# Optimization experiments

Hardware: AMD Instinct MI355X
Metric: run time of the kernel (lower is better)

## Reference

```python
import jax, jax.numpy as jnp
import numpy as np

N_NODES = 50000
D_IN = 128
D_OUT = 128
N_EDGES = 800000


def setup_inputs() -> dict:
    key = jax.random.key(0)
    ks = jax.random.split(key, 6)
    x = jax.random.normal(ks[0], (N_NODES, D_IN), dtype=jnp.float32)
    # xavier-uniform-ish init for the per-support weights
    limit = float(np.sqrt(6.0 / (D_IN + D_OUT)))
    weights = jax.random.uniform(ks[1], (2, D_IN, D_OUT), dtype=jnp.float32,
                                 minval=-limit, maxval=limit)
    edge_idx0 = jax.random.randint(ks[2], (2, N_EDGES), 0, N_NODES, dtype=jnp.int64 if jax.config.jax_enable_x64 else jnp.int32)
    vals0 = jax.random.uniform(ks[3], (N_EDGES,), dtype=jnp.float32)
    edge_idx1 = jax.random.randint(ks[4], (2, N_EDGES), 0, N_NODES, dtype=jnp.int64 if jax.config.jax_enable_x64 else jnp.int32)
    vals1 = jax.random.uniform(ks[5], (N_EDGES,), dtype=jnp.float32)
    return {"x": x, "weights": weights, "edge_idx0": edge_idx0, "vals0": vals0,
            "edge_idx1": edge_idx1, "vals1": vals1}


def _spmm(edge_idx, vals, dense, n_rows):
    # (sparse COO A) @ dense : out[row] += vals * dense[col]
    rows, cols = edge_idx[0], edge_idx[1]
    gathered = dense[cols] * vals[:, None]  # [E, D_OUT]
    return jax.ops.segment_sum(gathered, rows, num_segments=n_rows)


def reference(x, weights, edge_idx0, vals0, edge_idx1, vals1):
    n = x.shape[0]
    out = jnp.zeros((n, D_OUT), dtype=x.dtype)
    for w, ei, v in ((weights[0], edge_idx0, vals0), (weights[1], edge_idx1, vals1)):
        pre_sup = x @ w                       # [N, D_OUT] dense GEMM
        out = out + _spmm(ei, v, pre_sup, n)  # SpMM accumulate
    return jax.nn.relu(out)
```

## Files before the change

kernel.cpp:

```cpp
#include <hip/hip_runtime.h>

#define N_NODES 50000
#define D 128
#define N_EDGES 800000
#define SCAN_BLOCKS ((N_NODES + 255) / 256)
#define GEMM_BLOCKS ((N_NODES + 63) / 64)
#define BINS 196
#define NB1 256
#define CH1 3125
#define NKEY 2048

typedef __attribute__((ext_vector_type(8))) short short8;
typedef __attribute__((ext_vector_type(4))) float f32x4;

__device__ __forceinline__ unsigned short f2bf(float f) {
    unsigned u = __builtin_bit_cast(unsigned, f);
    u += 0x7FFFu + ((u >> 16) & 1u);
    return (unsigned short)(u >> 16);
}
__device__ __forceinline__ float bflo(unsigned p) {
    return __builtin_bit_cast(float, p << 16);
}
__device__ __forceinline__ float bfhi(unsigned p) {
    return __builtin_bit_cast(float, p & 0xFFFF0000u);
}

__global__ __launch_bounds__(256) void wt_build(const float* __restrict__ w,
                                                unsigned short* __restrict__ wt) {
    int i = blockIdx.x * 256 + threadIdx.x;
    if (i < 2 * D * D) {
        int s = i >> 14, rem = i & 16383, c = rem >> 7, k = rem & 127;
        wt[i] = f2bf(w[s * D * D + k * D + c]);
    }
}

template<int NS>
__device__ __forceinline__ void gemm_body(const float* __restrict__ x,
                                          const unsigned short* __restrict__ wt,
                                          unsigned short* __restrict__ pre0,
                                          unsigned short* __restrict__ pre1,
                                          int n_rows, int blk) {
    const int lane = threadIdx.x & 63;
    const int wid  = threadIdx.x >> 6;
    const int q    = lane >> 4;
    const int rlo  = lane & 15;
    const int r0   = blk * 64 + wid * 16;
    if (r0 >= n_rows) return;

    const float4* x4 = (const float4*)x;
    int arow  = r0 + rlo;
    int arowc = arow < n_rows ? arow : n_rows - 1;

    short8 afr[4];
    #pragma unroll
    for (int kb = 0; kb < 4; ++kb) {
        float4 fa = x4[(size_t)arowc * 32 + kb * 8 + q * 2];
        float4 fb = x4[(size_t)arowc * 32 + kb * 8 + q * 2 + 1];
        short8 a;
        a[0] = (short)f2bf(fa.x); a[1] = (short)f2bf(fa.y);
        a[2] = (short)f2bf(fa.z); a[3] = (short)f2bf(fa.w);
        a[4] = (short)f2bf(fb.x); a[5] = (short)f2bf(fb.y);
        a[6] = (short)f2bf(fb.z); a[7] = (short)f2bf(fb.w);
        afr[kb] = a;
    }

    const short8* wt8 = (const short8*)wt;
    f32x4 acc[NS][8];
    #pragma unroll
    for (int s = 0; s < NS; ++s)
        #pragma unroll
        for (int t = 0; t < 8; ++t)
            acc[s][t] = (f32x4){0.f, 0.f, 0.f, 0.f};

    #pragma unroll
    for (int t = 0; t < 8; ++t) {
        int c = t * 16 + rlo;
        #pragma unroll
        for (int kb = 0; kb < 4; ++kb) {
            short8 b0 = wt8[(size_t)c * 16 + kb * 4 + q];
            acc[0][t] = __builtin_amdgcn_mfma_f32_16x16x32_bf16(afr[kb], b0, acc[0][t], 0, 0, 0);
            if (NS == 2) {
                short8 b1 = wt8[(size_t)(D + c) * 16 + kb * 4 + q];
                acc[1][t] = __builtin_amdgcn_mfma_f32_16x16x32_bf16(afr[kb], b1, acc[1][t], 0, 0, 0);
            }
        }
    }

    #pragma unroll
    for (int i = 0; i < 4; ++i) {
        int rw = r0 + q * 4 + i;
        if (rw < n_rows) {
            #pragma unroll
            for (int t = 0; t < 8; ++t) {
                pre0[(size_t)rw * D + t * 16 + rlo] = f2bf(acc[0][t][i]);
                if (NS == 2) pre1[(size_t)rw * D + t * 16 + rlo] = f2bf(acc[1][t][i]);
            }
        }
    }
}


__global__ __launch_bounds__(256) void p1_count(const int* __restrict__ r0,
                                                const int* __restrict__ r1,
                                                int* __restrict__ h) {
    int s = blockIdx.y, blk = blockIdx.x;
    const int* r = s ? r1 : r0;
    __shared__ int hist[BINS];
    for (int i = threadIdx.x; i < BINS; i += 256) hist[i] = 0;
    __syncthreads();
    int start = blk * CH1, end = start + CH1;
    for (int e = start + (int)threadIdx.x; e < end; e += 256)
        atomicAdd(&hist[r[e] >> 8], 1);
    __syncthreads();
    for (int i = threadIdx.x; i < BINS; i += 256)
        h[(size_t)(s * NB1 + blk) * BINS + i] = hist[i];
}

__global__ __launch_bounds__(256) void binred(const int* __restrict__ h,
                                              int* __restrict__ bintot) {
    int s = blockIdx.y, bin = blockIdx.x, t = threadIdx.x;
    int v = h[(size_t)(s * NB1 + t) * BINS + bin];
    const int lane = t & 63, wid = t >> 6;
    __shared__ int ws[4];
    #pragma unroll
    for (int o = 32; o > 0; o >>= 1) v += __shfl_down(v, o);
    if (lane == 0) ws[wid] = v;
    __syncthreads();
    if (t == 0) bintot[s * BINS + bin] = ws[0] + ws[1] + ws[2] + ws[3];
}

__global__ __launch_bounds__(256) void binscan(const int* __restrict__ bintot,
                                               int* __restrict__ binbase) {
    int s = blockIdx.x, t = threadIdx.x;
    int v = (t < BINS) ? bintot[s * BINS + t] : 0;
    const int lane = t & 63, wid = t >> 6;
    __shared__ int ws[4];
    int incl = v;
    #pragma unroll
    for (int o = 1; o < 64; o <<= 1) { int tv = __shfl_up(incl, o); if (lane >= o) incl += tv; }
    if (lane == 63) ws[wid] = incl;
    __syncthreads();
    int wbase = 0;
    #pragma unroll
    for (int j = 0; j < 4; ++j) wbase += (j < wid) ? ws[j] : 0;
    int excl = wbase + incl - v;
    if (t < BINS) binbase[s * (BINS + 1) + t] = excl;
    if (t == BINS - 1) binbase[s * (BINS + 1) + BINS] = excl + v;
}

__global__ __launch_bounds__(256) void blkscan(int* __restrict__ h,
                                               const int* __restrict__ binbase) {
    int s = blockIdx.y, bin = blockIdx.x, t = threadIdx.x;
    size_t idx = (size_t)(s * NB1 + t) * BINS + bin;
    int v = h[idx];
    const int lane = t & 63, wid = t >> 6;
    __shared__ int ws[4];
    int incl = v;
    #pragma unroll
    for (int o = 1; o < 64; o <<= 1) { int tv = __shfl_up(incl, o); if (lane >= o) incl += tv; }
    if (lane == 63) ws[wid] = incl;
    __syncthreads();
    int wbase = 0;
    #pragma unroll
    for (int j = 0; j < 4; ++j) wbase += (j < wid) ? ws[j] : 0;
    h[idx] = binbase[s * (BINS + 1) + bin] + (wbase + incl - v);
}

__global__ __launch_bounds__(256) void k_fill_gemm(const float* __restrict__ x,
                                                   const unsigned short* __restrict__ wt,
                                                   unsigned short* __restrict__ pre0,
                                                   unsigned short* __restrict__ pre1,
                                                   const int* __restrict__ r0, const int* __restrict__ c0,
                                                   const float* __restrict__ v0,
                                                   const int* __restrict__ r1, const int* __restrict__ c1,
                                                   const float* __restrict__ v1,
                                                   const int* __restrict__ h,
                                                   int2* __restrict__ rec, int n_rows) {
    int bid = blockIdx.x;
    if (bid < 2 * NB1) {
        int s = bid & 1, blk = bid >> 1;
        const int*   r = s ? r1 : r0;
        const int*   c = s ? c1 : c0;
        const float* v = s ? v1 : v0;
        int2* rs = rec + (size_t)s * N_EDGES;
        __shared__ int base[BINS];
        __shared__ int cnt2[BINS];
        for (int i = threadIdx.x; i < BINS; i += 256) {
            base[i] = h[(size_t)(s * NB1 + blk) * BINS + i];
            cnt2[i] = 0;
        }
        __syncthreads();
        int start = blk * CH1, end = start + CH1;
        for (int e = start + (int)threadIdx.x; e < end; e += 256) {
            int rr = r[e], cc = c[e];
            float vv = v[e];
            int bin = rr >> 8;
            int lr = atomicAdd(&cnt2[bin], 1);
            rs[base[bin] + lr] = make_int2((cc << 8) | (rr & 255), __float_as_int(vv));
        }
    } else {
        gemm_body<2>(x, wt, pre0, pre1, n_rows, bid - 2 * NB1);
    }
}

__global__ __launch_bounds__(512) void p2_sort(const int* __restrict__ binbase,
                                               const int2* __restrict__ rec,
                                               unsigned* __restrict__ ep,
                                               int* __restrict__ off) {
    int s = blockIdx.y, bin = blockIdx.x, t = threadIdx.x;
    int bs  = binbase[s * (BINS + 1) + bin];
    int be  = binbase[s * (BINS + 1) + bin + 1];
    int cnt = be - bs;
    const int2* rs = rec + (size_t)s * N_EDGES;
    unsigned* es = ep + (size_t)s * N_EDGES;
    __shared__ int lc[NKEY];
    __shared__ int cur[NKEY];
    __shared__ int ws[8];
    #pragma unroll
    for (int j = 0; j < NKEY / 512; ++j) lc[t + j * 512] = 0;
    __syncthreads();
    for (int i = t; i < cnt; i += 512) {
        int2 R = rs[bs + i];
        int col = R.x >> 8;
        int key = ((R.x & 255) << 3) | (col >> 13);
        atomicAdd(&lc[key], 1);
    }
    __syncthreads();
    int kb = t * 4;
    int s0 = lc[kb], s1 = lc[kb + 1], s2 = lc[kb + 2], s3 = lc[kb + 3];
    int tot = s0 + s1 + s2 + s3;
    const int lane = t & 63, wid = t >> 6;
    int incl = tot;
    #pragma unroll
    for (int o = 1; o < 64; o <<= 1) { int tv = __shfl_up(incl, o); if (lane >= o) incl += tv; }
    if (lane == 63) ws[wid] = incl;
    __syncthreads();
    int wbase = 0;
    #pragma unroll
    for (int j = 0; j < 8; ++j) wbase += (j < wid) ? ws[j] : 0;
    int excl = wbase + incl - tot;
    cur[kb]     = excl;
    cur[kb + 1] = excl + s0;
    cur[kb + 2] = excl + s0 + s1;
    cur[kb + 3] = excl + s0 + s1 + s2;
    if ((t & 1) == 0) {
        int row = bin * 256 + (t >> 1);
        if (row < N_NODES) off[s * (N_NODES + 1) + row] = bs + excl;
    }
    if (bin == 0 && t == 0) off[s * (N_NODES + 1) + N_NODES] = N_EDGES;
    __syncthreads();
    for (int i = t; i < cnt; i += 512) {
        int2 R = rs[bs + i];
        int col = R.x >> 8;
        int key = ((R.x & 255) << 3) | (col >> 13);
        int p = atomicAdd(&cur[key], 1);
        es[bs + p] = ((unsigned)col << 16) | (unsigned)f2bf(__int_as_float(R.y));
    }
}

__device__ __forceinline__ void row_acc4(const unsigned* __restrict__ ep,
                                         const unsigned* __restrict__ prew,
                                         int b, int e, int lane, float& ax, float& ay) {
    int i = b;
    for (; i + 7 < e; i += 8) {
        unsigned E[8], P[8];
        #pragma unroll
        for (int j = 0; j < 8; ++j) E[j] = ep[i + j];
        #pragma unroll
        for (int j = 0; j < 8; ++j) P[j] = prew[(size_t)(E[j] >> 16) * 64 + lane];
        #pragma unroll
        for (int j = 0; j < 8; ++j) {
            float w = bflo(E[j]);
            ax = fmaf(w, bflo(P[j]), ax);
            ay = fmaf(w, bfhi(P[j]), ay);
        }
    }
    if (i + 3 < e) {
        unsigned E[4], P[4];
        #pragma unroll
        for (int j = 0; j < 4; ++j) E[j] = ep[i + j];
        #pragma unroll
        for (int j = 0; j < 4; ++j) P[j] = prew[(size_t)(E[j] >> 16) * 64 + lane];
        #pragma unroll
        for (int j = 0; j < 4; ++j) {
            float w = bflo(E[j]);
            ax = fmaf(w, bflo(P[j]), ax);
            ay = fmaf(w, bfhi(P[j]), ay);
        }
        i += 4;
    }
    for (; i < e; ++i) {
        unsigned E = ep[i];
        float w = bflo(E);
        unsigned p = prew[(size_t)(E >> 16) * 64 + lane];
        ax = fmaf(w, bflo(p), ax);
        ay = fmaf(w, bfhi(p), ay);
    }
}

__global__ __launch_bounds__(256) void gather_fused4(const int* __restrict__ off_base,
                                                     const unsigned* __restrict__ ep_base,
                                                     const unsigned short* __restrict__ pre0,
                                                     const unsigned short* __restrict__ pre1,
                                                     float* __restrict__ out, int n_rows) {
    const int lane = threadIdx.x & 63;
    const int wid  = threadIdx.x >> 6;
    const int wpg  = 4 * gridDim.x;
    const unsigned* ep1b = ep_base + N_EDGES;
    const int* o1 = off_base + (N_NODES + 1);
    const unsigned* pre0w = (const unsigned*)pre0;
    const unsigned* pre1w = (const unsigned*)pre1;
    float2* out2 = (float2*)out;
    for (int r = blockIdx.x * 4 + wid; r < n_rows; r += wpg) {
        float ax0 = 0.f, ay0 = 0.f, ax1 = 0.f, ay1 = 0.f;
        int i0 = off_base[r], e0 = off_base[r + 1];
        int i1 = o1[r],       e1 = o1[r + 1];
        while (i0 + 7 < e0 && i1 + 7 < e1) {
            unsigned E0[8], E1[8], P0[8], P1[8];
            #pragma unroll
            for (int j = 0; j < 8; ++j) { E0[j] = ep_base[i0 + j]; E1[j] = ep1b[i1 + j]; }
            #pragma unroll
            for (int j = 0; j < 8; ++j) {
                P0[j] = pre0w[(size_t)(E0[j] >> 16) * 64 + lane];
                P1[j] = pre1w[(size_t)(E1[j] >> 16) * 64 + lane];
            }
            #pragma unroll
            for (int j = 0; j < 8; ++j) {
                float w0 = bflo(E0[j]);
                float w1 = bflo(E1[j]);
                ax0 = fmaf(w0, bflo(P0[j]), ax0);
                ay0 = fmaf(w0, bfhi(P0[j]), ay0);
                ax1 = fmaf(w1, bflo(P1[j]), ax1);
                ay1 = fmaf(w1, bfhi(P1[j]), ay1);
            }
            i0 += 8; i1 += 8;
        }
        row_acc4(ep_base, pre0w, i0, e0, lane, ax0, ay0);
        row_acc4(ep1b,    pre1w, i1, e1, lane, ax1, ay1);
        float2 o;
        o.x = fmaxf(ax0 + ax1, 0.f);
        o.y = fmaxf(ay0 + ay1, 0.f);
        out2[(size_t)r * 64 + lane] = o;
    }
}

__device__ __forceinline__ void row_acc(const int2* __restrict__ ep,
                                        const unsigned short* __restrict__ pre,
                                        int b, int e, int lane, float& ax, float& ay) {
    int i = b;
    for (; i + 7 < e; i += 8) {
        int2 E[8];
        unsigned P[8];
        #pragma unroll
        for (int j = 0; j < 8; ++j) E[j] = ep[i + j];
        #pragma unroll
        for (int j = 0; j < 8; ++j) P[j] = *(const unsigned*)(pre + (size_t)E[j].x * D + 2 * lane);
        #pragma unroll
        for (int j = 0; j < 8; ++j) {
            float w = __int_as_float(E[j].y);
            ax = fmaf(w, bflo(P[j]), ax);
            ay = fmaf(w, bfhi(P[j]), ay);
        }
    }
    for (; i < e; ++i) {
        int2 e0 = ep[i];
        float w = __int_as_float(e0.y);
        unsigned p = *(const unsigned*)(pre + (size_t)e0.x * D + 2 * lane);
        ax = fmaf(w, bflo(p), ax);
        ay = fmaf(w, bfhi(p), ay);
    }
}

__global__ __launch_bounds__(256) void gather_fused(const int* __restrict__ off_base,
                                                    const int2* __restrict__ ep_base,
                                                    const unsigned short* __restrict__ pre0,
                                                    const unsigned short* __restrict__ pre1,
                                                    float* __restrict__ out, int n_rows) {
    const int lane = threadIdx.x & 63;
    const int wid  = threadIdx.x >> 6;
    const int wpg  = 4 * gridDim.x;
    const int2* ep1b = ep_base + N_EDGES;
    const int* o1 = off_base + (N_NODES + 1);
    float2* out2 = (float2*)out;
    for (int r = blockIdx.x * 4 + wid; r < n_rows; r += wpg) {
        float ax0 = 0.f, ay0 = 0.f, ax1 = 0.f, ay1 = 0.f;
        row_acc(ep_base, pre0, off_base[r], off_base[r + 1], lane, ax0, ay0);
        row_acc(ep1b,    pre1, o1[r], o1[r + 1], lane, ax1, ay1);
        float2 o;
        o.x = fmaxf(ax0 + ax1, 0.f);
        o.y = fmaxf(ay0 + ay1, 0.f);
        out2[(size_t)r * 64 + lane] = o;
    }
}

__global__ __launch_bounds__(256) void gemm_mfma2(const float* __restrict__ x,
                                                  const unsigned short* __restrict__ wt,
                                                  unsigned short* __restrict__ pre0,
                                                  unsigned short* __restrict__ pre1, int n_rows) {
    gemm_body<2>(x, wt, pre0, pre1, n_rows, blockIdx.x);
}
__global__ __launch_bounds__(256) void gemm_mfma1(const float* __restrict__ x,
                                                  const unsigned short* __restrict__ wt,
                                                  unsigned short* __restrict__ pre, int n_rows) {
    gemm_body<1>(x, wt, pre, pre, n_rows, blockIdx.x);
}

__global__ __launch_bounds__(256) void hist_rank(const int* __restrict__ r0,
                                                 const int* __restrict__ r1,
                                                 int* __restrict__ cnt_base,
                                                 int* __restrict__ rank_base, int n_edges) {
    int s = blockIdx.y;
    const int* r = s ? r1 : r0;
    int* cnt  = cnt_base + s * N_NODES;
    int* rank = rank_base + (size_t)s * N_EDGES;
    for (int e = blockIdx.x * 256 + threadIdx.x; e < n_edges; e += gridDim.x * 256)
        rank[e] = atomicAdd(&cnt[r[e]], 1);
}

__global__ __launch_bounds__(256) void scanA(const int* __restrict__ cnt_base,
                                             int* __restrict__ bsum) {
    int s = blockIdx.y;
    int i = blockIdx.x * 256 + threadIdx.x;
    int v = (i < N_NODES) ? cnt_base[s * N_NODES + i] : 0;
    const int lane = threadIdx.x & 63;
    const int wid  = threadIdx.x >> 6;
    __shared__ int ws[4];
    #pragma unroll
    for (int off = 32; off > 0; off >>= 1) v += __shfl_down(v, off);
    if (lane == 0) ws[wid] = v;
    __syncthreads();
    if (threadIdx.x == 0)
        bsum[s * SCAN_BLOCKS + blockIdx.x] = ws[0] + ws[1] + ws[2] + ws[3];
}

__global__ __launch_bounds__(256) void scanC2(const int* __restrict__ cnt_base,
                                              const int* __restrict__ bsum,
                                              int* __restrict__ off_base) {
    int s = blockIdx.y;
    int t = threadIdx.x;
    const int lane = t & 63;
    const int wid  = t >> 6;
    __shared__ int ws[4];
    __shared__ int base_s;
    int bv = (t < (int)blockIdx.x && t < SCAN_BLOCKS) ? bsum[s * SCAN_BLOCKS + t] : 0;
    #pragma unroll
    for (int off = 32; off > 0; off >>= 1) bv += __shfl_down(bv, off);
    if (lane == 0) ws[wid] = bv;
    __syncthreads();
    if (t == 0) base_s = ws[0] + ws[1] + ws[2] + ws[3];
    __syncthreads();
    int base = base_s;
    __syncthreads();
    int i = blockIdx.x * 256 + t;
    int v = (i < N_NODES) ? cnt_base[s * N_NODES + i] : 0;
    int incl = v;
    #pragma unroll
    for (int off = 1; off < 64; off <<= 1) {
        int tv = __shfl_up(incl, off);
        if (lane >= off) incl += tv;
    }
    if (lane == 63) ws[wid] = incl;
    __syncthreads();
    int wbase = 0;
    #pragma unroll
    for (int j = 0; j < 4; ++j) wbase += (j < wid) ? ws[j] : 0;
    int* off = off_base + s * (N_NODES + 1);
    if (i < N_NODES)
        off[i] = base + wbase + incl - v;
    if (blockIdx.x == 0 && t == 0)
        off[N_NODES] = N_EDGES;
}

__global__ __launch_bounds__(256) void scatter_csr(const int* __restrict__ r0, const int* __restrict__ c0,
                                                   const float* __restrict__ v0,
                                                   const int* __restrict__ r1, const int* __restrict__ c1,
                                                   const float* __restrict__ v1,
                                                   const int* __restrict__ off_base,
                                                   const int* __restrict__ rank_base,
                                                   int2* __restrict__ ep_base, int n_edges) {
    int s = blockIdx.y;
    const int*   r    = s ? r1 : r0;
    const int*   c    = s ? c1 : c0;
    const float* v    = s ? v1 : v0;
    const int*   off  = off_base + s * (N_NODES + 1);
    const int*   rank = rank_base + (size_t)s * N_EDGES;
    int2* ep = ep_base + (size_t)s * N_EDGES;
    for (int e = blockIdx.x * 256 + threadIdx.x; e < n_edges; e += gridDim.x * 256) {
        int p = off[r[e]] + rank[e];
        int2 rec;
        rec.x = c[e];
        rec.y = __float_as_int(v[e]);
        ep[p] = rec;
    }
}

template<int ACCUM_RELU>
__global__ __launch_bounds__(256) void gather_one(const int* __restrict__ off,
                                                  const int2* __restrict__ ep,
                                                  const unsigned short* __restrict__ pre,
                                                  float* __restrict__ out, int n_rows) {
    const int lane = threadIdx.x & 63;
    const int wid  = threadIdx.x >> 6;
    const int wpg  = 4 * gridDim.x;
    float2* out2 = (float2*)out;
    for (int r = blockIdx.x * 4 + wid; r < n_rows; r += wpg) {
        float ax = 0.f, ay = 0.f;
        row_acc(ep, pre, off[r], off[r + 1], lane, ax, ay);
        float2 o;
        if (ACCUM_RELU) {
            float2 prev = out2[(size_t)r * 64 + lane];
            o.x = fmaxf(prev.x + ax, 0.f);
            o.y = fmaxf(prev.y + ay, 0.f);
        } else {
            o.x = ax; o.y = ay;
        }
        out2[(size_t)r * 64 + lane] = o;
    }
}

extern "C" void kernel_launch(void* const* d_in, const int* in_sizes, int n_in,
                              void* d_out, int out_size, void* d_ws, size_t ws_size,
                              hipStream_t stream) {
    const float* x       = (const float*)d_in[0];
    const float* weights = (const float*)d_in[1];
    const int*   ei0     = (const int*)d_in[2];
    const float* v0      = (const float*)d_in[3];
    const int*   ei1     = (const int*)d_in[4];
    const float* v1      = (const float*)d_in[5];
    float* out = (float*)d_out;

    dim3 blk(256);
    const size_t PRE_B = (size_t)N_NODES * D * sizeof(unsigned short);
    const size_t WT_B  = (size_t)2 * D * D * sizeof(unsigned short);
    const size_t H_B   = (size_t)2 * NB1 * BINS * 4;
    const size_t BT_B  = (size_t)2 * BINS * 4;
    const size_t BB_B  = (size_t)2 * (BINS + 1) * 4;
    const size_t OFF_B = (size_t)2 * (N_NODES + 1) * 4;
    const size_t E8    = (size_t)2 * N_EDGES * sizeof(int2);
    const size_t E4    = (size_t)2 * N_EDGES * 4;

    char* wsb = (char*)d_ws;
    size_t needNew = 2 * PRE_B + WT_B + H_B + BT_B + BB_B + OFF_B + E8 + E4;
    size_t needA1 = 2 * PRE_B + WT_B
                  + (size_t)(2 * (N_NODES + 1) + 2 * N_NODES + 2 * SCAN_BLOCKS) * 4
                  + E8 + (size_t)2 * N_EDGES * 4;

    if (ws_size >= needNew) {
        unsigned short* pre0 = (unsigned short*)wsb;
        unsigned short* pre1 = (unsigned short*)(wsb + PRE_B);
        unsigned short* wt   = (unsigned short*)(wsb + 2 * PRE_B);
        int*  h       = (int*)(wsb + 2 * PRE_B + WT_B);
        int*  bintot  = (int*)((char*)h + H_B);
        int*  binbase = (int*)((char*)bintot + BT_B);
        int*  off     = (int*)((char*)binbase + BB_B);
        int2* rec     = (int2*)((char*)off + OFF_B);
        unsigned* ep  = (unsigned*)(rec + (size_t)2 * N_EDGES);

        wt_build<<<128, blk, 0, stream>>>(weights, wt);
        p1_count<<<dim3(NB1, 2), blk, 0, stream>>>(ei0, ei1, h);
        binred  <<<dim3(BINS, 2), blk, 0, stream>>>(h, bintot);
        binscan <<<2, blk, 0, stream>>>(bintot, binbase);
        blkscan <<<dim3(BINS, 2), blk, 0, stream>>>(h, binbase);
        k_fill_gemm<<<2 * NB1 + GEMM_BLOCKS, blk, 0, stream>>>(
            x, wt, pre0, pre1,
            ei0, ei0 + N_EDGES, v0, ei1, ei1 + N_EDGES, v1,
            h, rec, N_NODES);
        p2_sort<<<dim3(BINS, 2), dim3(512), 0, stream>>>(binbase, rec, ep, off);
        gather_fused4<<<12500, blk, 0, stream>>>(off, ep, pre0, pre1, out, N_NODES);
    } else if (ws_size >= needA1) {
        unsigned short* pre0 = (unsigned short*)wsb;
        unsigned short* pre1 = (unsigned short*)(wsb + PRE_B);
        unsigned short* wt   = (unsigned short*)(wsb + 2 * PRE_B);
        int*  off  = (int*)(wsb + 2 * PRE_B + WT_B);
        int*  cnt  = off + 2 * (N_NODES + 1);
        int*  bsum = cnt + 2 * N_NODES;
        int2* ep   = (int2*)(bsum + 2 * SCAN_BLOCKS);
        int*  rank = (int*)(ep + (size_t)2 * N_EDGES);

        hipMemsetAsync(cnt, 0, (size_t)2 * N_NODES * sizeof(int), stream);
        wt_build<<<128, blk, 0, stream>>>(weights, wt);
        hist_rank<<<dim3(1024, 2), blk, 0, stream>>>(ei0, ei1, cnt, rank, N_EDGES);
        gemm_mfma2<<<GEMM_BLOCKS, blk, 0, stream>>>(x, wt, pre0, pre1, N_NODES);
        scanA<<<dim3(SCAN_BLOCKS, 2), blk, 0, stream>>>(cnt, bsum);
        scanC2<<<dim3(SCAN_BLOCKS, 2), blk, 0, stream>>>(cnt, bsum, off);
        scatter_csr<<<dim3(1024, 2), blk, 0, stream>>>(ei0, ei0 + N_EDGES, v0,
                                                       ei1, ei1 + N_EDGES, v1,
                                                       off, rank, ep, N_EDGES);
        gather_fused<<<12500, blk, 0, stream>>>(off, ep, pre0, pre1, out, N_NODES);
    } else {
        unsigned short* pre = (unsigned short*)wsb;
        unsigned short* wt  = (unsigned short*)(wsb + PRE_B);
        int*  off  = (int*)(wsb + PRE_B + WT_B);
        int*  cnt  = off + (N_NODES + 1);
        int*  bsum = cnt + N_NODES;
        int2* ep   = (int2*)(bsum + SCAN_BLOCKS);
        int*  rank = (int*)pre;

        wt_build<<<128, blk, 0, stream>>>(weights, wt);
        const int* rows[2] = {ei0, ei1};
        const int* cols[2] = {ei0 + N_EDGES, ei1 + N_EDGES};
        const float* vals[2] = {v0, v1};
        for (int s = 0; s < 2; ++s) {
            hipMemsetAsync(cnt, 0, (size_t)N_NODES * sizeof(int), stream);
            hist_rank<<<dim3(1024, 1), blk, 0, stream>>>(rows[s], rows[s], cnt, rank, N_EDGES);
            scanA<<<dim3(SCAN_BLOCKS, 1), blk, 0, stream>>>(cnt, bsum);
            scanC2<<<dim3(SCAN_BLOCKS, 1), blk, 0, stream>>>(cnt, bsum, off);
            scatter_csr<<<dim3(1024, 1), blk, 0, stream>>>(rows[s], cols[s], vals[s],
                                                           rows[s], cols[s], vals[s],
                                                           off, rank, ep, N_EDGES);
            gemm_mfma1<<<GEMM_BLOCKS, blk, 0, stream>>>(x, wt + (size_t)s * D * D, pre, N_NODES);
            if (s == 0)
                gather_one<0><<<12500, blk, 0, stream>>>(off, ep, pre, out, N_NODES);
            else
                gather_one<1><<<12500, blk, 0, stream>>>(off, ep, pre, out, N_NODES);
        }
    }
}
```

Measured before the change: 141.3 us.

## Fuse bin reduction and scan, split GEMM support loops, scalarize gather offsets

Merges the binred and binscan kernels into one two-block kernel that sums the per-block histograms serially per bin, then scans them, removing one launch and the bintot buffer. The GEMM inner loop is split so the second support's MFMAs run in a separate loop instead of being interleaved with the first. In the gather kernel, the row offsets are read through readfirstlane so they sit in scalar registers and the loop bounds are wave-uniform. The fused reduction runs on only two blocks with serial strided loads, so it trades parallelism for one fewer launch.

```diff
diff --git a/kernel.cpp b/kernel.cpp
--- a/kernel.cpp
+++ b/kernel.cpp
@@ -79,7 +79,14 @@
         for (int kb = 0; kb < 4; ++kb) {
             short8 b0 = wt8[(size_t)c * 16 + kb * 4 + q];
             acc[0][t] = __builtin_amdgcn_mfma_f32_16x16x32_bf16(afr[kb], b0, acc[0][t], 0, 0, 0);
-            if (NS == 2) {
+        }
+    }
+    if (NS == 2) {
+        #pragma unroll
+        for (int t = 0; t < 8; ++t) {
+            int c = t * 16 + rlo;
+            #pragma unroll
+            for (int kb = 0; kb < 4; ++kb) {
                 short8 b1 = wt8[(size_t)(D + c) * 16 + kb * 4 + q];
                 acc[1][t] = __builtin_amdgcn_mfma_f32_16x16x32_bf16(afr[kb], b1, acc[1][t], 0, 0, 0);
             }
@@ -116,23 +123,18 @@
         h[(size_t)(s * NB1 + blk) * BINS + i] = hist[i];
 }
 
-__global__ __launch_bounds__(256) void binred(const int* __restrict__ h,
-                                              int* __restrict__ bintot) {
-    int s = blockIdx.y, bin = blockIdx.x, t = threadIdx.x;
-    int v = h[(size_t)(s * NB1 + t) * BINS + bin];
-    const int lane = t & 63, wid = t >> 6;
-    __shared__ int ws[4];
-    #pragma unroll
-    for (int o = 32; o > 0; o >>= 1) v += __shfl_down(v, o);
-    if (lane == 0) ws[wid] = v;
-    __syncthreads();
-    if (t == 0) bintot[s * BINS + bin] = ws[0] + ws[1] + ws[2] + ws[3];
-}
-
-__global__ __launch_bounds__(256) void binscan(const int* __restrict__ bintot,
-                                               int* __restrict__ binbase) {
+__global__ __launch_bounds__(256) void binredscan(const int* __restrict__ h,
+                                                  int* __restrict__ binbase) {
     int s = blockIdx.x, t = threadIdx.x;
-    int v = (t < BINS) ? bintot[s * BINS + t] : 0;
+    int acc[8] = {0, 0, 0, 0, 0, 0, 0, 0};
+    if (t < BINS) {
+        for (int blk = 0; blk < NB1; blk += 8) {
+            #pragma unroll
+            for (int j = 0; j < 8; ++j)
+                acc[j] += h[(size_t)(s * NB1 + blk + j) * BINS + t];
+        }
+    }
+    int v = acc[0] + acc[1] + acc[2] + acc[3] + acc[4] + acc[5] + acc[6] + acc[7];
     const int lane = t & 63, wid = t >> 6;
     __shared__ int ws[4];
     int incl = v;
@@ -313,8 +315,10 @@
     float2* out2 = (float2*)out;
     for (int r = blockIdx.x * 4 + wid; r < n_rows; r += wpg) {
         float ax0 = 0.f, ay0 = 0.f, ax1 = 0.f, ay1 = 0.f;
-        int i0 = off_base[r], e0 = off_base[r + 1];
-        int i1 = o1[r],       e1 = o1[r + 1];
+        int i0 = __builtin_amdgcn_readfirstlane(off_base[r]);
+        int e0 = __builtin_amdgcn_readfirstlane(off_base[r + 1]);
+        int i1 = __builtin_amdgcn_readfirstlane(o1[r]);
+        int e1 = __builtin_amdgcn_readfirstlane(o1[r + 1]);
         while (i0 + 7 < e0 && i1 + 7 < e1) {
             unsigned E0[8], E1[8], P0[8], P1[8];
             #pragma unroll
@@ -533,14 +537,13 @@
     const size_t PRE_B = (size_t)N_NODES * D * sizeof(unsigned short);
     const size_t WT_B  = (size_t)2 * D * D * sizeof(unsigned short);
     const size_t H_B   = (size_t)2 * NB1 * BINS * 4;
-    const size_t BT_B  = (size_t)2 * BINS * 4;
     const size_t BB_B  = (size_t)2 * (BINS + 1) * 4;
     const size_t OFF_B = (size_t)2 * (N_NODES + 1) * 4;
     const size_t E8    = (size_t)2 * N_EDGES * sizeof(int2);
     const size_t E4    = (size_t)2 * N_EDGES * 4;
 
     char* wsb = (char*)d_ws;
-    size_t needNew = 2 * PRE_B + WT_B + H_B + BT_B + BB_B + OFF_B + E8 + E4;
+    size_t needNew = 2 * PRE_B + WT_B + H_B + BB_B + OFF_B + E8 + E4;
     size_t needA1 = 2 * PRE_B + WT_B
                   + (size_t)(2 * (N_NODES + 1) + 2 * N_NODES + 2 * SCAN_BLOCKS) * 4
                   + E8 + (size_t)2 * N_EDGES * 4;
@@ -550,17 +553,15 @@
         unsigned short* pre1 = (unsigned short*)(wsb + PRE_B);
         unsigned short* wt   = (unsigned short*)(wsb + 2 * PRE_B);
         int*  h       = (int*)(wsb + 2 * PRE_B + WT_B);
-        int*  bintot  = (int*)((char*)h + H_B);
-        int*  binbase = (int*)((char*)bintot + BT_B);
+        int*  binbase = (int*)((char*)h + H_B);
         int*  off     = (int*)((char*)binbase + BB_B);
         int2* rec     = (int2*)((char*)off + OFF_B);
         unsigned* ep  = (unsigned*)(rec + (size_t)2 * N_EDGES);
 
         wt_build<<<128, blk, 0, stream>>>(weights, wt);
         p1_count<<<dim3(NB1, 2), blk, 0, stream>>>(ei0, ei1, h);
-        binred  <<<dim3(BINS, 2), blk, 0, stream>>>(h, bintot);
-        binscan <<<2, blk, 0, stream>>>(bintot, binbase);
-        blkscan <<<dim3(BINS, 2), blk, 0, stream>>>(h, binbase);
+        binredscan<<<2, blk, 0, stream>>>(h, binbase);
+        blkscan<<<dim3(BINS, 2), blk, 0, stream>>>(h, binbase);
         k_fill_gemm<<<2 * NB1 + GEMM_BLOCKS, blk, 0, stream>>>(
             x, wt, pre0, pre1,
             ei0, ei0 + N_EDGES, v0, ei1, ei1 + N_EDGES, v1,
```

After: 142.9 us. No clear change (+1.1%).
